# Performance work log

Measured on AMD Instinct MI355X. Metric: run time of the kernel, lower is better.

The kernel has to match this reference:

```python
import jax, jax.numpy as jnp
import numpy as np
import math

DIM = 2048
D_STATE = 64
EXPAND = 2
CHUNK = 64
HEADDIM = 64
D_CONV = 4
D_INNER = EXPAND * DIM          # 4096
NHEADS = D_INNER // HEADDIM     # 64


def _segsum(x):
    """x: (..., T) -> (..., T, T); out[i,j] = sum_{k=j+1}^{i} x[k] for i>=j else -inf."""
    T = x.shape[-1]
    keep = jnp.tril(jnp.ones((T, T), bool), -1)          # strictly lower
    seg = jnp.cumsum(jnp.where(keep, x[..., None], 0.0), axis=-2)
    valid = jnp.tril(jnp.ones((T, T), bool))
    return jnp.where(valid, seg, -jnp.inf)


def _ssd(X, A, B, C, block):
    """Chunkwise SSD scan (Mamba-2 Listing 1). X:(b,L,h,p) A:(b,L,h) B,C:(b,L,h,n)."""
    b, L, h, p = X.shape
    n = B.shape[-1]
    c = L // block
    X = X.reshape(b, c, block, h, p)
    A = A.reshape(b, c, block, h)
    B = B.reshape(b, c, block, h, n)
    C = C.reshape(b, c, block, h, n)
    A = jnp.transpose(A, (0, 3, 1, 2))                    # (b,h,c,l)
    A_cum = jnp.cumsum(A, axis=-1)
    # intra-chunk (diagonal block) output
    L_intra = jnp.exp(_segsum(A))                         # (b,h,c,l,s)
    Y_diag = jnp.einsum('bclhn,bcshn,bhcls,bcshp->bclhp', C, B, L_intra, X)
    # per-chunk final states
    decay_states = jnp.exp(A_cum[..., -1:] - A_cum)       # (b,h,c,l)
    states = jnp.einsum('bclhn,bhcl,bclhp->bchpn', B, decay_states, X)
    states = jnp.concatenate([jnp.zeros_like(states[:, :1]), states], axis=1)
    # inter-chunk recurrence across chunk boundaries
    chunk_end = jnp.pad(A_cum[..., -1], ((0, 0), (0, 0), (1, 0)))  # (b,h,c+1)
    decay_chunk = jnp.exp(_segsum(chunk_end))             # (b,h,c+1,c+1)
    new_states = jnp.einsum('bhzc,bchpn->bzhpn', decay_chunk, states)
    states_per_chunk = new_states[:, :-1]
    # off-diagonal contribution from carried-in states
    state_decay_out = jnp.exp(A_cum)                      # (b,h,c,l)
    Y_off = jnp.einsum('bclhn,bchpn,bhcl->bclhp', C, states_per_chunk, state_decay_out)
    return (Y_diag + Y_off).reshape(b, L, h, p)


def setup_inputs() -> dict:
    key = jax.random.key(0)
    ks = jax.random.split(key, 6)
    b, l = 2, 2048
    x = jax.random.normal(ks[0], (b, l, DIM), jnp.float32)
    proj_out = 2 * D_INNER + 2 * D_STATE + NHEADS
    in_proj_w = jax.random.normal(ks[1], (proj_out, DIM), jnp.float32) / math.sqrt(DIM)
    conv_w = jax.random.normal(ks[2], (D_INNER, 1, D_CONV), jnp.float32) / math.sqrt(D_CONV)
    conv_b = jnp.zeros((D_INNER,), jnp.float32)
    out_proj_w = jax.random.normal(ks[3], (DIM, D_INNER), jnp.float32) / math.sqrt(D_INNER)
    A_log = jnp.zeros((NHEADS,), jnp.float32)
    D_skip = jnp.ones((D_INNER,), jnp.float32)
    u = jax.random.uniform(ks[4], (NHEADS,), jnp.float32)
    dt = jnp.clip(jnp.exp(u * (math.log(0.1) - math.log(0.001)) + math.log(0.001)), 1e-4, None)
    dt_bias = dt + jnp.log(-jnp.expm1(-dt))
    return dict(x=x, in_proj_w=in_proj_w, conv_w=conv_w, conv_b=conv_b,
                out_proj_w=out_proj_w, A_log=A_log, D_skip=D_skip, dt_bias=dt_bias)


def reference(x, in_proj_w, conv_w, conv_b, out_proj_w, A_log, D_skip, dt_bias):
    b, l, _ = x.shape
    proj = x @ in_proj_w.T
    splits = [D_INNER, 2 * D_INNER, 2 * D_INNER + D_STATE, 2 * D_INNER + 2 * D_STATE]
    x_branch, z, B_in, C_in, dt = jnp.split(proj, splits, axis=-1)
    # causal depthwise conv1d (torch pads both sides then slices [:l] == left-pad only)
    xc = jnp.transpose(x_branch, (0, 2, 1))               # (b, d_inner, l)
    xc = jax.lax.conv_general_dilated(
        xc, conv_w, (1,), [(D_CONV - 1, 0)],
        dimension_numbers=('NCH', 'OIH', 'NCH'), feature_group_count=D_INNER)
    xc = xc + conv_b[None, :, None]
    x_act = jax.nn.silu(jnp.transpose(xc, (0, 2, 1)))     # (b,l,d_inner)
    x_h = x_act.reshape(b, l, NHEADS, HEADDIM)
    dt_f = jax.nn.softplus(dt + dt_bias)                  # (b,l,h)
    A_f = -jnp.exp(A_log)                                 # (h,)
    X_disc = x_h * dt_f[..., None]
    A_disc = A_f[None, None, :] * dt_f
    B_b = jnp.broadcast_to(B_in[:, :, None, :], (b, l, NHEADS, D_STATE))
    C_b = jnp.broadcast_to(C_in[:, :, None, :], (b, l, NHEADS, D_STATE))
    Y = _ssd(X_disc, A_disc, B_b, C_b, CHUNK)             # (b,l,h,p)
    y = Y.reshape(b, l, D_INNER) + D_skip * x_act
    y = y * jax.nn.silu(z)
    return y @ out_proj_w.T
```

## Files before the change

### kernel.cpp

```cpp
#include <hip/hip_runtime.h>

typedef unsigned short u16;
typedef unsigned int   u32;
typedef __attribute__((ext_vector_type(8))) short bf16x8;
typedef __attribute__((ext_vector_type(4))) float f32x4;

__device__ __forceinline__ u16 f2bf(float f){
  u32 u = __builtin_bit_cast(u32, f);
  u32 r = (u + 0x7FFFu + ((u >> 16) & 1u)) >> 16;
  return (u16)r;
}
__device__ __forceinline__ float bf2f(u16 h){
  u32 u = ((u32)h) << 16;
  return __builtin_bit_cast(float, u);
}
__device__ __forceinline__ void llds16(const u16* g, u16* l){
  __builtin_amdgcn_global_load_lds((const __attribute__((address_space(1))) void*)g,
                                   (__attribute__((address_space(3))) void*)l, 16, 0, 0);
}

#define FENCE asm volatile("" ::: "memory")
#define BAR   do { FENCE; __builtin_amdgcn_s_barrier(); FENCE; } while (0)
#define LGKM0 do { asm volatile("s_waitcnt lgkmcnt(0)" ::: "memory"); __builtin_amdgcn_sched_barrier(0); } while (0)
#define VMC6  do { asm volatile("s_waitcnt vmcnt(6)" ::: "memory"); __builtin_amdgcn_sched_barrier(0); } while (0)
#define VMC0  do { asm volatile("s_waitcnt vmcnt(0)" ::: "memory"); __builtin_amdgcn_sched_barrier(0); } while (0)

#define MFMAQ(mh, nh)                                                         \
  _Pragma("unroll") for (int i = 0; i < 4; i++)                               \
    _Pragma("unroll") for (int j = 0; j < 2; j++)                             \
      _Pragma("unroll") for (int kb = 0; kb < 2; kb++)                        \
        acc[mh][nh][i][j] = __builtin_amdgcn_mfma_f32_16x16x32_bf16(          \
            a[i][kb], bfr[j][kb], acc[mh][nh][i][j], 0, 0, 0);

__global__ __launch_bounds__(256) void cast4(const float* __restrict__ in, u16* __restrict__ out, int n4){
  int i = blockIdx.x * 256 + threadIdx.x;
  if (i >= n4) return;
  float4 v = ((const float4*)in)[i];
  u32 lo = (u32)f2bf(v.x) | ((u32)f2bf(v.y) << 16);
  u32 hi = (u32)f2bf(v.z) | ((u32)f2bf(v.w) << 16);
  ((uint2*)out)[i] = make_uint2(lo, hi);
}

__global__ __launch_bounds__(256) void castpad_w1(const float* __restrict__ in, u16* __restrict__ out){
  int i = blockIdx.x * 256 + threadIdx.x;
  if (i >= 8448 * 512) return;
  int nrow = i >> 9;
  float4 v = make_float4(0.f, 0.f, 0.f, 0.f);
  if (nrow < 8384) v = ((const float4*)in)[i];
  u32 lo = (u32)f2bf(v.x) | ((u32)f2bf(v.y) << 16);
  u32 hi = (u32)f2bf(v.z) | ((u32)f2bf(v.w) << 16);
  ((uint2*)out)[i] = make_uint2(lo, hi);
}

__global__ __launch_bounds__(256)
void gemm128(const u16* __restrict__ A, const u16* __restrict__ Bm, u16* __restrict__ Cout,
             int NYT, int N, int K)
{
  __shared__ u16 As[8192], Bs[8192];
  const int tid = threadIdx.x;
  const int lane = tid & 63, wave = tid >> 6;
  const int wm = (wave >> 1) * 64, wn = (wave & 1) * 64;
  const int lr = lane & 15, lk8 = (lane >> 4) * 8;
  const int lterm = lr * 32 + (lk8 ^ ((lr & 8) << 1));
  const int nwg = gridDim.x;
  const int lid = blockIdx.x;
  const int q = nwg >> 3;
  const int swz = (lid & 7) * q + (lid >> 3);
  const int ty = swz % NYT, tx = swz / NYT;
  const size_t bm0 = (size_t)ty * 128;
  const size_t bn0 = (size_t)tx * 128;
  const int cg = (lane & 3) ^ ((lane & 32) ? 2 : 0);
  const int rsub = lane >> 2;
  const int ag0 = (wave >> 1) * 8;
  const int bg0 = (wave & 1) * 8;

  f32x4 acc[4][4] = {};

  for (int k0 = 0; k0 < K; k0 += 64) {
    __syncthreads();
    #pragma unroll
    for (int u = 0; u < 4; u++) {
      const int si = wave * 4 + u;
      const int row = (si >> 1) * 16 + rsub;
      const int kc = (si & 1) * 32 + cg * 8;
      llds16(A  + (bm0 + row) * (size_t)K + k0 + kc, As + si * 512 + lane * 8);
      llds16(Bm + (bn0 + row) * (size_t)K + k0 + kc, Bs + si * 512 + lane * 8);
    }
    __syncthreads();
    #pragma unroll
    for (int kb = 0; kb < 2; kb++) {
      bf16x8 af[4], bfv[4];
      #pragma unroll
      for (int m = 0; m < 4; m++) af[m]  = *(const bf16x8*)&As[(ag0 + m * 2 + kb) * 512 + lterm];
      #pragma unroll
      for (int n = 0; n < 4; n++) bfv[n] = *(const bf16x8*)&Bs[(bg0 + n * 2 + kb) * 512 + lterm];
      #pragma unroll
      for (int m = 0; m < 4; m++)
        #pragma unroll
        for (int n = 0; n < 4; n++)
          acc[m][n] = __builtin_amdgcn_mfma_f32_16x16x32_bf16(af[m], bfv[n], acc[m][n], 0, 0, 0);
    }
  }

  const int lg = (lane >> 4) * 4;
  #pragma unroll
  for (int m = 0; m < 4; m++)
    #pragma unroll
    for (int n = 0; n < 4; n++) {
      size_t col = bn0 + wn + n * 16 + lr;
      #pragma unroll
      for (int j = 0; j < 4; j++) {
        size_t row = bm0 + wm + m * 16 + lg + j;
        Cout[row * N + col] = f2bf(acc[m][n][j]);
      }
    }
}

__global__ __launch_bounds__(512, 2)
void gemm2sk(const u16* __restrict__ A, const u16* __restrict__ Bm, float* __restrict__ P,
             int NYT, int N, int KLEN, int LDK)
{
  __shared__ u16 L[65536];
  const int tid = threadIdx.x;
  const int lane = tid & 63, wid = tid >> 6;
  const int wr = wid >> 2, wc = wid & 3;
  const int lr = lane & 15, lk8 = (lane >> 4) * 8;
  const int lterm = lr * 32 + (lk8 ^ ((lr & 8) << 1));
  const int lid = blockIdx.x;
  const int ks = lid >> 7;
  const int lid2 = lid & 127;
  const int q = 128 >> 3;
  const int swz = (lid2 & 7) * q + (lid2 >> 3);
  const int ty = swz % NYT, tx = swz / NYT;
  const size_t bm0 = (size_t)ty * 256;
  const size_t bn0 = (size_t)tx * 256;
  const int NT = KLEN >> 6;
  const size_t koff = (size_t)ks * KLEN;
  float* Pout = P + (size_t)ks * 8388608;

  const int si0 = wid * 2, si1 = si0 + 1;
  const int rsub = lane >> 2;
  const int cg = (lane & 3) ^ ((lane & 32) ? 2 : 0);
  const int rh0 = (si0 >> 1) * 16 + rsub, kc0 = (si0 & 1) * 32 + cg * 8;
  const int rh1 = (si1 >> 1) * 16 + rsub, kc1 = (si1 & 1) * 32 + cg * 8;

  auto stage = [&](int isA, int h, int tt) {
    const int slot = (tt & 1) * 4 + (isA ? 0 : 2) + h;
    const u16* gb = (isA ? A : Bm) + ((isA ? bm0 : bn0) + (size_t)h * 128) * (size_t)LDK + koff;
    u16* lb = L + slot * 8192 + lane * 8;
    llds16(gb + (size_t)rh0 * LDK + (size_t)tt * 64 + kc0, lb + si0 * 512);
    llds16(gb + (size_t)rh1 * LDK + (size_t)tt * 64 + kc1, lb + si1 * 512);
  };

  bf16x8 a[4][2], bfr[2][2];
  f32x4 acc[2][2][4][2] = {};

  auto rdA = [&](int p, int mh) {
    #pragma unroll
    for (int i = 0; i < 4; i++)
      #pragma unroll
      for (int kb = 0; kb < 2; kb++)
        a[i][kb] = *(const bf16x8*)&L[(p * 4 + mh) * 8192 + ((wr * 4 + i) * 2 + kb) * 512 + lterm];
  };
  auto rdB = [&](int p, int nh) {
    #pragma unroll
    for (int j = 0; j < 2; j++)
      #pragma unroll
      for (int kb = 0; kb < 2; kb++)
        bfr[j][kb] = *(const bf16x8*)&L[(p * 4 + 2 + nh) * 8192 + ((wc * 2 + j) * 2 + kb) * 512 + lterm];
  };

  stage(1, 0, 0); stage(1, 1, 0); stage(0, 0, 0); stage(0, 1, 0);
  stage(1, 0, 1); stage(1, 1, 1); stage(0, 0, 1);
  VMC6;
  BAR;

  for (int t = 0; t < NT; ++t) {
    const int p = t & 1;
    const bool s1 = (t + 1 < NT);
    const bool s2 = (t + 2 < NT);
    rdA(p, 0); rdB(p, 0);
    if (s1) stage(0, 1, t + 1);
    BAR; LGKM0;
    __builtin_amdgcn_s_setprio(1); MFMAQ(0, 0); __builtin_amdgcn_s_setprio(0);
    BAR;
    rdB(p, 1);
    if (s2) stage(1, 0, t + 2);
    BAR; LGKM0;
    __builtin_amdgcn_s_setprio(1); MFMAQ(0, 1); __builtin_amdgcn_s_setprio(0);
    BAR;
    rdA(p, 1); rdB(p, 0);
    BAR; LGKM0;
    __builtin_amdgcn_s_setprio(1); MFMAQ(1, 0); __builtin_amdgcn_s_setprio(0);
    BAR;
    rdB(p, 1);
    if (s2) { stage(1, 1, t + 2); stage(0, 0, t + 2); }
    if (t < NT - 2) { VMC6; } else { VMC0; }
    BAR; LGKM0;
    __builtin_amdgcn_s_setprio(1); MFMAQ(1, 1); __builtin_amdgcn_s_setprio(0);
    BAR;
  }

  const int lg4 = (lane >> 4) * 4;
  #pragma unroll
  for (int mh = 0; mh < 2; mh++)
    #pragma unroll
    for (int nh = 0; nh < 2; nh++)
      #pragma unroll
      for (int i = 0; i < 4; i++)
        #pragma unroll
        for (int j = 0; j < 2; j++) {
          size_t col = bn0 + nh * 128 + wc * 32 + j * 16 + lr;
          #pragma unroll
          for (int r2 = 0; r2 < 4; r2++) {
            size_t row = bm0 + mh * 128 + wr * 64 + i * 16 + lg4 + r2;
            Pout[row * N + col] = acc[mh][nh][i][j][r2];
          }
        }
}

__global__ __launch_bounds__(256)
void addp(const float* __restrict__ p0, const float* __restrict__ p1, float* __restrict__ out){
  int i = blockIdx.x * 256 + threadIdx.x;
  float4 a = ((const float4*)p0)[i];
  float4 b = ((const float4*)p1)[i];
  ((float4*)out)[i] = make_float4(a.x + b.x, a.y + b.y, a.z + b.z, a.w + b.w);
}

__global__ __launch_bounds__(256)
void postproj(const u16* __restrict__ proj, const float* __restrict__ dt_bias,
              float* __restrict__ dtf, u16* __restrict__ Bb, u16* __restrict__ Cb)
{
  int i = blockIdx.x * 256 + threadIdx.x;
  if (i >= 4096 * 64) return;
  int bl = i >> 6, hh = i & 63;
  const u16* pr = proj + (size_t)bl * 8448;
  float dv = bf2f(pr[8320 + hh]) + dt_bias[hh];
  dtf[i] = dv > 20.f ? dv : log1pf(__expf(dv));
  Bb[i] = pr[8192 + hh];
  Cb[i] = pr[8256 + hh];
}

__global__ __launch_bounds__(256)
void conv_silu(const u16* __restrict__ proj, const float* __restrict__ cw,
               const float* __restrict__ cb, const float* __restrict__ dtf,
               u16* __restrict__ xact, u16* __restrict__ Xd)
{
  const int g = blockIdx.x;
  const int bl0 = g * 4;
  const int l0 = bl0 & 2047;
  const int d0 = blockIdx.y * 2048 + threadIdx.x * 8;
  const int hd = d0 >> 6;
  float4 wv[8];
  #pragma unroll
  for (int e = 0; e < 8; e++) wv[e] = *(const float4*)&cw[(size_t)(d0 + e) * 4];
  float bias[8];
  {
    float4 b0 = *(const float4*)&cb[d0];
    float4 b1 = *(const float4*)&cb[d0 + 4];
    bias[0]=b0.x; bias[1]=b0.y; bias[2]=b0.z; bias[3]=b0.w;
    bias[4]=b1.x; bias[5]=b1.y; bias[6]=b1.z; bias[7]=b1.w;
  }
  float r[7][8];
  #pragma unroll
  for (int t = 0; t < 7; t++) {
    const int l = l0 - 3 + t;
    if (l >= 0) {
      uint4 rv = *(const uint4*)(proj + (size_t)(bl0 - 3 + t) * 8448 + d0);
      const u16* re = (const u16*)&rv;
      #pragma unroll
      for (int e = 0; e < 8; e++) r[t][e] = bf2f(re[e]);
    } else {
      #pragma unroll
      for (int e = 0; e < 8; e++) r[t][e] = 0.f;
    }
  }
  #pragma unroll
  for (int lo = 0; lo < 4; lo++) {
    const float dt = dtf[(size_t)(bl0 + lo) * 64 + hd];
    u16 xo[8], xdo[8];
    #pragma unroll
    for (int e = 0; e < 8; e++) {
      float v = bias[e] + wv[e].x * r[lo][e] + wv[e].y * r[lo + 1][e]
                        + wv[e].z * r[lo + 2][e] + wv[e].w * r[lo + 3][e];
      float sil = v / (1.f + __expf(-v));
      xo[e]  = f2bf(sil);
      xdo[e] = f2bf(sil * dt);
    }
    *(uint4*)(xact + (size_t)(bl0 + lo) * 4096 + d0) = *(const uint4*)xo;
    *(uint4*)(Xd   + (size_t)(bl0 + lo) * 4096 + d0) = *(const uint4*)xdo;
  }
}

__global__ __launch_bounds__(256)
void ssd_states(const u16* __restrict__ Xd, const u16* __restrict__ Bg,
                const float* __restrict__ dtf, const float* __restrict__ A_log,
                u16* __restrict__ Stg, float* __restrict__ dtot)
{
  const int wg = blockIdx.x;
  const int b = wg >> 11, h = wg & 63;
  const int c = (wg >> 6) & 31;
  const int bl0 = b * 2048 + c * 64;
  __shared__ u16 Bt[64*64], Xts[64*64];
  __shared__ float avals[64], Acum[64], Adec[64];
  const int tid = threadIdx.x, wave = tid >> 6, lane = tid & 63;
  const int qi = (wave >> 1) * 32, qj = (wave & 1) * 32;
  const int lr = lane & 15, lk8 = (lane >> 4) * 8, lg = (lane >> 4) * 4;
  const float negA = -__expf(A_log[h]);

  if (tid < 64) avals[tid] = negA * dtf[(size_t)(bl0 + tid) * 64 + h];
  __syncthreads();
  if (tid < 64) { float s = 0.f; for (int j = 0; j <= tid; j++) s += avals[j]; Acum[tid] = s; }
  __syncthreads();
  if (tid < 64) Adec[tid] = __expf(Acum[63] - Acum[tid]);
  if (tid == 0) dtot[wg] = __expf(Acum[63]);
  __syncthreads();
  {
    int s = tid & 63, c0 = (tid >> 6) * 16;
    float dec = Adec[s];
    const u16* bs = Bg + (size_t)(bl0 + s) * 64 + c0;
    const u16* xs = Xd + (size_t)(bl0 + s) * 4096 + h * 64 + c0;
    #pragma unroll
    for (int j = 0; j < 16; j++) {
      Bt[(c0 + j) * 64 + s] = bs[j];
      Xts[(c0 + j) * 64 + s] = f2bf(bf2f(xs[j]) * dec);
    }
  }
  __syncthreads();
  f32x4 accst[2][2] = {};
  #pragma unroll
  for (int kk = 0; kk < 64; kk += 32) {
    bf16x8 xsf[2], btf[2];
    #pragma unroll
    for (int t = 0; t < 2; t++) {
      xsf[t] = *(const bf16x8*)&Xts[(qi + t * 16 + lr) * 64 + kk + lk8];
      btf[t] = *(const bf16x8*)&Bt [(qj + t * 16 + lr) * 64 + kk + lk8];
    }
    #pragma unroll
    for (int ti = 0; ti < 2; ti++)
      #pragma unroll
      for (int tj = 0; tj < 2; tj++)
        accst[ti][tj] = __builtin_amdgcn_mfma_f32_16x16x32_bf16(xsf[ti], btf[tj], accst[ti][tj], 0, 0, 0);
  }
  u16* So = Stg + (size_t)wg * 4096;
  #pragma unroll
  for (int ti = 0; ti < 2; ti++)
    #pragma unroll
    for (int tj = 0; tj < 2; tj++) {
      int nn = qj + tj * 16 + lr;
      #pragma unroll
      for (int r2 = 0; r2 < 4; r2++) {
        int pp = qi + ti * 16 + lg + r2;
        So[pp * 64 + nn] = f2bf(accst[ti][tj][r2]);
      }
    }
}

__global__ __launch_bounds__(256)
void ssd_scan(u16* __restrict__ Stg, const float* __restrict__ dtot)
{
  const int gid = blockIdx.x * 256 + threadIdx.x;
  const int bh = gid >> 12;
  const int pn = gid & 4095;
  const int b = bh >> 6, h = bh & 63;
  float R = 0.f;
  for (int c = 0; c < 32; ++c) {
    const int whc = b * 2048 + c * 64 + h;
    size_t idx = (size_t)whc * 4096 + pn;
    float st = bf2f(Stg[idx]);
    Stg[idx] = f2bf(R);
    R = R * dtot[whc] + st;
  }
}

__global__ __launch_bounds__(256)
void ssd_y(const u16* __restrict__ Xd, const u16* __restrict__ Bg, const u16* __restrict__ Cg,
           const float* __restrict__ dtf, const float* __restrict__ A_log,
           const u16* __restrict__ xact, const u16* __restrict__ proj,
           const float* __restrict__ Dskip, const u16* __restrict__ Stg,
           u16* __restrict__ Yout)
{
  const int wg = blockIdx.x;
  const int b = wg >> 11, h = wg & 63;
  const int c = (wg >> 6) & 31;
  const int bl0 = b * 2048 + c * 64;
  __shared__ u16 Cb[64*64], Bb[64*64], Xt[64*64], Sb[64*64], P[64*64];
  __shared__ float avals[64], Acum[64], Aexp[64];
  const int tid = threadIdx.x, wave = tid >> 6, lane = tid & 63;
  const int qi = (wave >> 1) * 32, qj = (wave & 1) * 32;
  const int lr = lane & 15, lk8 = (lane >> 4) * 8, lg = (lane >> 4) * 4;
  const float negA = -__expf(A_log[h]);

  if (tid < 64) avals[tid] = negA * dtf[(size_t)(bl0 + tid) * 64 + h];
  __syncthreads();
  if (tid < 64) { float s = 0.f; for (int j = 0; j <= tid; j++) s += avals[j]; Acum[tid] = s; }
  __syncthreads();
  if (tid < 64) Aexp[tid] = __expf(Acum[tid]);
  __syncthreads();
  {
    int l = tid >> 2, n0 = (tid & 3) * 16;
    const uint4* s0 = (const uint4*)(Cg + (size_t)(bl0 + l) * 64 + n0);
    *(uint4*)&Cb[l * 64 + n0] = s0[0]; *(uint4*)&Cb[l * 64 + n0 + 8] = s0[1];
    const uint4* s1 = (const uint4*)(Bg + (size_t)(bl0 + l) * 64 + n0);
    *(uint4*)&Bb[l * 64 + n0] = s1[0]; *(uint4*)&Bb[l * 64 + n0 + 8] = s1[1];
    int s = tid & 63, c0 = (tid >> 6) * 16;
    const u16* xs = Xd + (size_t)(bl0 + s) * 4096 + h * 64 + c0;
    #pragma unroll
    for (int j = 0; j < 16; j++) Xt[(c0 + j) * 64 + s] = xs[j];
    const uint4* sp = (const uint4*)(Stg + (size_t)wg * 4096 + tid * 16);
    *(uint4*)&Sb[tid * 16] = sp[0]; *(uint4*)&Sb[tid * 16 + 8] = sp[1];
  }
  __syncthreads();
  f32x4 accs[2][2] = {}; f32x4 accy[2][2] = {};
  #pragma unroll
  for (int kk = 0; kk < 64; kk += 32) {
    bf16x8 cf[2], bfr[2], sf[2];
    #pragma unroll
    for (int t = 0; t < 2; t++) {
      cf[t]  = *(const bf16x8*)&Cb[(qi + t * 16 + lr) * 64 + kk + lk8];
      bfr[t] = *(const bf16x8*)&Bb[(qj + t * 16 + lr) * 64 + kk + lk8];
      sf[t]  = *(const bf16x8*)&Sb[(qj + t * 16 + lr) * 64 + kk + lk8];
    }
    #pragma unroll
    for (int ti = 0; ti < 2; ti++)
      #pragma unroll
      for (int tj = 0; tj < 2; tj++) {
        accs[ti][tj] = __builtin_amdgcn_mfma_f32_16x16x32_bf16(cf[ti], bfr[tj], accs[ti][tj], 0, 0, 0);
        accy[ti][tj] = __builtin_amdgcn_mfma_f32_16x16x32_bf16(cf[ti], sf[tj],  accy[ti][tj], 0, 0, 0);
      }
  }
  #pragma unroll
  for (int ti = 0; ti < 2; ti++)
    #pragma unroll
    for (int tj = 0; tj < 2; tj++) {
      int j = qj + tj * 16 + lr;
      float Aj = Acum[j];
      #pragma unroll
      for (int r2 = 0; r2 < 4; r2++) {
        int i = qi + ti * 16 + lg + r2;
        float v = (i >= j) ? accs[ti][tj][r2] * __expf(Acum[i] - Aj) : 0.f;
        P[i * 64 + j] = f2bf(v);
        accy[ti][tj][r2] *= Aexp[i];
      }
    }
  __syncthreads();
  #pragma unroll
  for (int kk = 0; kk < 64; kk += 32) {
    bf16x8 pf[2], xf_[2];
    #pragma unroll
    for (int t = 0; t < 2; t++) {
      pf[t]  = *(const bf16x8*)&P [(qi + t * 16 + lr) * 64 + kk + lk8];
      xf_[t] = *(const bf16x8*)&Xt[(qj + t * 16 + lr) * 64 + kk + lk8];
    }
    #pragma unroll
    for (int ti = 0; ti < 2; ti++)
      #pragma unroll
      for (int tj = 0; tj < 2; tj++)
        accy[ti][tj] = __builtin_amdgcn_mfma_f32_16x16x32_bf16(pf[ti], xf_[tj], accy[ti][tj], 0, 0, 0);
  }
  #pragma unroll
  for (int ti = 0; ti < 2; ti++)
    #pragma unroll
    for (int tj = 0; tj < 2; tj++) {
      int pcol = qj + tj * 16 + lr;
      int d = h * 64 + pcol;
      float dsk = Dskip[d];
      #pragma unroll
      for (int r2 = 0; r2 < 4; r2++) {
        int lrow = qi + ti * 16 + lg + r2;
        size_t bl = (size_t)bl0 + lrow;
        float y = accy[ti][tj][r2];
        float xa = bf2f(xact[bl * 4096 + d]);
        float z = bf2f(proj[bl * 8448 + 4096 + d]);
        float sz = z / (1.f + __expf(-z));
        Yout[bl * 4096 + d] = f2bf((y + dsk * xa) * sz);
      }
    }
}

__global__ __launch_bounds__(256)
void ssd_kernel(const u16* __restrict__ Xd, const u16* __restrict__ Bg, const u16* __restrict__ Cg,
                const float* __restrict__ dtf, const float* __restrict__ A_log,
                const u16* __restrict__ xact, const u16* __restrict__ proj,
                const float* __restrict__ Dskip, u16* __restrict__ Yout)
{
  const int bh = blockIdx.x;
  const int b = bh >> 6, h = bh & 63;
  __shared__ float S[64 * 64];
  __shared__ u16 Cb[64*64], Bb[64*64], Bt[64*64], Xt[64*64], Xts[64*64], Sb[64*64], P[64*64];
  __shared__ float avals[64], Acum[64], Adec[64], Aexp[64];
  const int tid = threadIdx.x, wave = tid >> 6, lane = tid & 63;
  const int qi = (wave >> 1) * 32, qj = (wave & 1) * 32;
  const int lr = lane & 15, lk8 = (lane >> 4) * 8, lg = (lane >> 4) * 4;
  const float negA = -__expf(A_log[h]);

  for (int i = tid; i < 4096; i += 256) S[i] = 0.f;

  for (int c = 0; c < 32; ++c) {
    const int bl0 = b * 2048 + c * 64;
    __syncthreads();
    if (tid < 64) avals[tid] = negA * dtf[(size_t)(bl0 + tid) * 64 + h];
    __syncthreads();
    if (tid < 64) { float s = 0.f; for (int j = 0; j <= tid; j++) s += avals[j]; Acum[tid] = s; }
    __syncthreads();
    if (tid < 64) { float At = Acum[63]; Adec[tid] = __expf(At - Acum[tid]); Aexp[tid] = __expf(Acum[tid]); }
    __syncthreads();
    {
      int l = tid >> 2, n0 = (tid & 3) * 16;
      const uint4* s0 = (const uint4*)(Cg + (size_t)(bl0 + l) * 64 + n0);
      *(uint4*)&Cb[l * 64 + n0] = s0[0]; *(uint4*)&Cb[l * 64 + n0 + 8] = s0[1];
      const uint4* s1 = (const uint4*)(Bg + (size_t)(bl0 + l) * 64 + n0);
      *(uint4*)&Bb[l * 64 + n0] = s1[0]; *(uint4*)&Bb[l * 64 + n0 + 8] = s1[1];
      int s = tid & 63, c0 = (tid >> 6) * 16;
      float dec = Adec[s];
      const u16* bs = Bg + (size_t)(bl0 + s) * 64 + c0;
      const u16* xs = Xd + (size_t)(bl0 + s) * 4096 + h * 64 + c0;
      #pragma unroll
      for (int j = 0; j < 16; j++) {
        Bt[(c0 + j) * 64 + s] = bs[j];
        u16 xv = xs[j];
        Xt[(c0 + j) * 64 + s] = xv;
        Xts[(c0 + j) * 64 + s] = f2bf(bf2f(xv) * dec);
      }
      int p = tid >> 2, m0 = (tid & 3) * 16;
      #pragma unroll
      for (int j = 0; j < 16; j++) Sb[p * 64 + m0 + j] = f2bf(S[p * 64 + m0 + j]);
    }
    __syncthreads();
    f32x4 accs[2][2] = {}; f32x4 accy[2][2] = {};
    #pragma unroll
    for (int kk = 0; kk < 64; kk += 32) {
      bf16x8 cf[2], bfr[2], sf[2];
      #pragma unroll
      for (int t = 0; t < 2; t++) {
        cf[t]  = *(const bf16x8*)&Cb[(qi + t * 16 + lr) * 64 + kk + lk8];
        bfr[t] = *(const bf16x8*)&Bb[(qj + t * 16 + lr) * 64 + kk + lk8];
        sf[t]  = *(const bf16x8*)&Sb[(qj + t * 16 + lr) * 64 + kk + lk8];
      }
      #pragma unroll
      for (int ti = 0; ti < 2; ti++)
        #pragma unroll
        for (int tj = 0; tj < 2; tj++) {
          accs[ti][tj] = __builtin_amdgcn_mfma_f32_16x16x32_bf16(cf[ti], bfr[tj], accs[ti][tj], 0, 0, 0);
          accy[ti][tj] = __builtin_amdgcn_mfma_f32_16x16x32_bf16(cf[ti], sf[tj],  accy[ti][tj], 0, 0, 0);
        }
    }
    #pragma unroll
    for (int ti = 0; ti < 2; ti++)
      #pragma unroll
      for (int tj = 0; tj < 2; tj++) {
        int j = qj + tj * 16 + lr;
        float Aj = Acum[j];
        #pragma unroll
        for (int r2 = 0; r2 < 4; r2++) {
          int i = qi + ti * 16 + lg + r2;
          float v = (i >= j) ? accs[ti][tj][r2] * __expf(Acum[i] - Aj) : 0.f;
          P[i * 64 + j] = f2bf(v);
          accy[ti][tj][r2] *= Aexp[i];
        }
      }
    __syncthreads();
    f32x4 accst[2][2] = {};
    #pragma unroll
    for (int kk = 0; kk < 64; kk += 32) {
      bf16x8 pf[2], xf_[2], xsf[2], btf[2];
      #pragma unroll
      for (int t = 0; t < 2; t++) {
        pf[t]  = *(const bf16x8*)&P  [(qi + t * 16 + lr) * 64 + kk + lk8];
        xf_[t] = *(const bf16x8*)&Xt [(qj + t * 16 + lr) * 64 + kk + lk8];
        xsf[t] = *(const bf16x8*)&Xts[(qi + t * 16 + lr) * 64 + kk + lk8];
        btf[t] = *(const bf16x8*)&Bt [(qj + t * 16 + lr) * 64 + kk + lk8];
      }
      #pragma unroll
      for (int ti = 0; ti < 2; ti++)
        #pragma unroll
        for (int tj = 0; tj < 2; tj++) {
          accy[ti][tj]  = __builtin_amdgcn_mfma_f32_16x16x32_bf16(pf[ti],  xf_[tj], accy[ti][tj],  0, 0, 0);
          accst[ti][tj] = __builtin_amdgcn_mfma_f32_16x16x32_bf16(xsf[ti], btf[tj], accst[ti][tj], 0, 0, 0);
        }
    }
    float dtot = Aexp[63];
    #pragma unroll
    for (int ti = 0; ti < 2; ti++)
      #pragma unroll
      for (int tj = 0; tj < 2; tj++) {
        int nn = qj + tj * 16 + lr;
        #pragma unroll
        for (int r2 = 0; r2 < 4; r2++) {
          int pp = qi + ti * 16 + lg + r2;
          int idx = pp * 64 + nn;
          S[idx] = dtot * S[idx] + accst[ti][tj][r2];
        }
      }
    #pragma unroll
    for (int ti = 0; ti < 2; ti++)
      #pragma unroll
      for (int tj = 0; tj < 2; tj++) {
        int pcol = qj + tj * 16 + lr;
        int d = h * 64 + pcol;
        float dsk = Dskip[d];
        #pragma unroll
        for (int r2 = 0; r2 < 4; r2++) {
          int lrow = qi + ti * 16 + lg + r2;
          size_t bl = (size_t)bl0 + lrow;
          float y = accy[ti][tj][r2];
          float xa = bf2f(xact[bl * 4096 + d]);
          float z = bf2f(proj[bl * 8448 + 4096 + d]);
          float sz = z / (1.f + __expf(-z));
          Yout[bl * 4096 + d] = f2bf((y + dsk * xa) * sz);
        }
      }
  }
}

extern "C" void kernel_launch(void* const* d_in, const int* in_sizes, int n_in,
                              void* d_out, int out_size, void* d_ws, size_t ws_size,
                              hipStream_t stream) {
  const float* x    = (const float*)d_in[0];
  const float* w1   = (const float*)d_in[1];
  const float* cw   = (const float*)d_in[2];
  const float* cbv  = (const float*)d_in[3];
  const float* w2   = (const float*)d_in[4];
  const float* alog = (const float*)d_in[5];
  const float* dsk  = (const float*)d_in[6];
  const float* dtb  = (const float*)d_in[7];
  float* out = (float*)d_out;

  char* ws = (char*)d_ws;
  u16*  x_bf  = (u16*)(ws + 0);
  u16*  w1p   = (u16*)(ws + 16777216);
  u16*  w2b   = (u16*)(ws + 51380224);
  u16*  proj  = (u16*)(ws + 68157440);
  float* dtf  = (float*)(ws + 137363456);
  u16*  Bbf   = (u16*)(ws + 138412032);
  u16*  Cbf   = (u16*)(ws + 138936320);
  u16*  xact  = (u16*)(ws + 139460608);
  u16*  Xdd   = (u16*)(ws + 173015040);
  u16*  yin   = (u16*)(ws + 206569472);
  u16*  Stg   = (u16*)(ws + 240123904);
  float* dtot = (float*)(ws + 273678336);
  const size_t NEED_PAR = 273694720ull;
  float* p0 = (float*)(ws + 68157440);
  float* p1 = p0 + 8388608;

  cast4<<<8192, 256, 0, stream>>>(x,  x_bf, 2097152);
  castpad_w1<<<16896, 256, 0, stream>>>(w1, w1p);
  cast4<<<8192, 256, 0, stream>>>(w2, w2b, 2097152);

  gemm128<<<2112, 256, 0, stream>>>(x_bf, w1p, proj, 32, 8448, 2048);

  postproj<<<1024, 256, 0, stream>>>(proj, dtb, dtf, Bbf, Cbf);
  conv_silu<<<dim3(1024, 2), 256, 0, stream>>>(proj, cw, cbv, dtf, xact, Xdd);

  if (ws_size >= NEED_PAR) {
    ssd_states<<<4096, 256, 0, stream>>>(Xdd, Bbf, dtf, alog, Stg, dtot);
    ssd_scan<<<2048, 256, 0, stream>>>(Stg, dtot);
    ssd_y<<<4096, 256, 0, stream>>>(Xdd, Bbf, Cbf, dtf, alog, xact, proj, dsk, Stg, yin);
  } else {
    ssd_kernel<<<128, 256, 0, stream>>>(Xdd, Bbf, Cbf, dtf, alog, xact, proj, dsk, yin);
  }

  gemm2sk<<<256, 512, 0, stream>>>(yin, w2b, p0, 16, 2048, 2048, 4096);
  addp<<<8192, 256, 0, stream>>>(p0, p1, out);
}
```

Before: 395.2 us.

## Replace split-K 256-tile out-proj GEMM and reduction with templated 128-tile GEMM

The output projection used a 256x256-tile split-K kernel writing two fp32 partials, followed by a separate add kernel. It now reuses the 128x128 gemm128 kernel, templated to write fp32 directly, with 512 blocks over the full K=4096. This removes the partial-sum writes, the extra reduction pass and one launch. The trade-off is giving up the larger tile and the more carefully pipelined schedule, with longer per-block K loops.

Result: slower. 413.5 us (+4.6%).

```diff
diff --git a/kernel.cpp b/kernel.cpp
--- a/kernel.cpp
+++ b/kernel.cpp
@@ -18,19 +18,6 @@
   __builtin_amdgcn_global_load_lds((const __attribute__((address_space(1))) void*)g,
                                    (__attribute__((address_space(3))) void*)l, 16, 0, 0);
 }
-
-#define FENCE asm volatile("" ::: "memory")
-#define BAR   do { FENCE; __builtin_amdgcn_s_barrier(); FENCE; } while (0)
-#define LGKM0 do { asm volatile("s_waitcnt lgkmcnt(0)" ::: "memory"); __builtin_amdgcn_sched_barrier(0); } while (0)
-#define VMC6  do { asm volatile("s_waitcnt vmcnt(6)" ::: "memory"); __builtin_amdgcn_sched_barrier(0); } while (0)
-#define VMC0  do { asm volatile("s_waitcnt vmcnt(0)" ::: "memory"); __builtin_amdgcn_sched_barrier(0); } while (0)
-
-#define MFMAQ(mh, nh)                                                         \
-  _Pragma("unroll") for (int i = 0; i < 4; i++)                               \
-    _Pragma("unroll") for (int j = 0; j < 2; j++)                             \
-      _Pragma("unroll") for (int kb = 0; kb < 2; kb++)                        \
-        acc[mh][nh][i][j] = __builtin_amdgcn_mfma_f32_16x16x32_bf16(          \
-            a[i][kb], bfr[j][kb], acc[mh][nh][i][j], 0, 0, 0);
 
 __global__ __launch_bounds__(256) void cast4(const float* __restrict__ in, u16* __restrict__ out, int n4){
   int i = blockIdx.x * 256 + threadIdx.x;
@@ -52,8 +39,9 @@
   ((uint2*)out)[i] = make_uint2(lo, hi);
 }
 
-__global__ __launch_bounds__(256)
-void gemm128(const u16* __restrict__ A, const u16* __restrict__ Bm, u16* __restrict__ Cout,
+template<bool OUTF32>
+__global__ __launch_bounds__(256)
+void gemm128(const u16* __restrict__ A, const u16* __restrict__ Bm, void* __restrict__ Cout,
              int NYT, int N, int K)
 {
   __shared__ u16 As[8192], Bs[8192];
@@ -111,120 +99,11 @@
       #pragma unroll
       for (int j = 0; j < 4; j++) {
         size_t row = bm0 + wm + m * 16 + lg + j;
-        Cout[row * N + col] = f2bf(acc[m][n][j]);
-      }
-    }
-}
-
-__global__ __launch_bounds__(512, 2)
-void gemm2sk(const u16* __restrict__ A, const u16* __restrict__ Bm, float* __restrict__ P,
-             int NYT, int N, int KLEN, int LDK)
-{
-  __shared__ u16 L[65536];
-  const int tid = threadIdx.x;
-  const int lane = tid & 63, wid = tid >> 6;
-  const int wr = wid >> 2, wc = wid & 3;
-  const int lr = lane & 15, lk8 = (lane >> 4) * 8;
-  const int lterm = lr * 32 + (lk8 ^ ((lr & 8) << 1));
-  const int lid = blockIdx.x;
-  const int ks = lid >> 7;
-  const int lid2 = lid & 127;
-  const int q = 128 >> 3;
-  const int swz = (lid2 & 7) * q + (lid2 >> 3);
-  const int ty = swz % NYT, tx = swz / NYT;
-  const size_t bm0 = (size_t)ty * 256;
-  const size_t bn0 = (size_t)tx * 256;
-  const int NT = KLEN >> 6;
-  const size_t koff = (size_t)ks * KLEN;
-  float* Pout = P + (size_t)ks * 8388608;
-
-  const int si0 = wid * 2, si1 = si0 + 1;
-  const int rsub = lane >> 2;
-  const int cg = (lane & 3) ^ ((lane & 32) ? 2 : 0);
-  const int rh0 = (si0 >> 1) * 16 + rsub, kc0 = (si0 & 1) * 32 + cg * 8;
-  const int rh1 = (si1 >> 1) * 16 + rsub, kc1 = (si1 & 1) * 32 + cg * 8;
-
-  auto stage = [&](int isA, int h, int tt) {
-    const int slot = (tt & 1) * 4 + (isA ? 0 : 2) + h;
-    const u16* gb = (isA ? A : Bm) + ((isA ? bm0 : bn0) + (size_t)h * 128) * (size_t)LDK + koff;
-    u16* lb = L + slot * 8192 + lane * 8;
-    llds16(gb + (size_t)rh0 * LDK + (size_t)tt * 64 + kc0, lb + si0 * 512);
-    llds16(gb + (size_t)rh1 * LDK + (size_t)tt * 64 + kc1, lb + si1 * 512);
-  };
-
-  bf16x8 a[4][2], bfr[2][2];
-  f32x4 acc[2][2][4][2] = {};
-
-  auto rdA = [&](int p, int mh) {
-    #pragma unroll
-    for (int i = 0; i < 4; i++)
-      #pragma unroll
-      for (int kb = 0; kb < 2; kb++)
-        a[i][kb] = *(const bf16x8*)&L[(p * 4 + mh) * 8192 + ((wr * 4 + i) * 2 + kb) * 512 + lterm];
-  };
-  auto rdB = [&](int p, int nh) {
-    #pragma unroll
-    for (int j = 0; j < 2; j++)
-      #pragma unroll
-      for (int kb = 0; kb < 2; kb++)
-        bfr[j][kb] = *(const bf16x8*)&L[(p * 4 + 2 + nh) * 8192 + ((wc * 2 + j) * 2 + kb) * 512 + lterm];
-  };
-
-  stage(1, 0, 0); stage(1, 1, 0); stage(0, 0, 0); stage(0, 1, 0);
-  stage(1, 0, 1); stage(1, 1, 1); stage(0, 0, 1);
-  VMC6;
-  BAR;
-
-  for (int t = 0; t < NT; ++t) {
-    const int p = t & 1;
-    const bool s1 = (t + 1 < NT);
-    const bool s2 = (t + 2 < NT);
-    rdA(p, 0); rdB(p, 0);
-    if (s1) stage(0, 1, t + 1);
-    BAR; LGKM0;
-    __builtin_amdgcn_s_setprio(1); MFMAQ(0, 0); __builtin_amdgcn_s_setprio(0);
-    BAR;
-    rdB(p, 1);
-    if (s2) stage(1, 0, t + 2);
-    BAR; LGKM0;
-    __builtin_amdgcn_s_setprio(1); MFMAQ(0, 1); __builtin_amdgcn_s_setprio(0);
-    BAR;
-    rdA(p, 1); rdB(p, 0);
-    BAR; LGKM0;
-    __builtin_amdgcn_s_setprio(1); MFMAQ(1, 0); __builtin_amdgcn_s_setprio(0);
-    BAR;
-    rdB(p, 1);
-    if (s2) { stage(1, 1, t + 2); stage(0, 0, t + 2); }
-    if (t < NT - 2) { VMC6; } else { VMC0; }
-    BAR; LGKM0;
-    __builtin_amdgcn_s_setprio(1); MFMAQ(1, 1); __builtin_amdgcn_s_setprio(0);
-    BAR;
-  }
-
-  const int lg4 = (lane >> 4) * 4;
-  #pragma unroll
-  for (int mh = 0; mh < 2; mh++)
-    #pragma unroll
-    for (int nh = 0; nh < 2; nh++)
-      #pragma unroll
-      for (int i = 0; i < 4; i++)
-        #pragma unroll
-        for (int j = 0; j < 2; j++) {
-          size_t col = bn0 + nh * 128 + wc * 32 + j * 16 + lr;
-          #pragma unroll
-          for (int r2 = 0; r2 < 4; r2++) {
-            size_t row = bm0 + mh * 128 + wr * 64 + i * 16 + lg4 + r2;
-            Pout[row * N + col] = acc[mh][nh][i][j][r2];
-          }
-        }
-}
-
-__global__ __launch_bounds__(256)
-void addp(const float* __restrict__ p0, const float* __restrict__ p1, float* __restrict__ out){
-  int i = blockIdx.x * 256 + threadIdx.x;
-  float4 a = ((const float4*)p0)[i];
-  float4 b = ((const float4*)p1)[i];
-  ((float4*)out)[i] = make_float4(a.x + b.x, a.y + b.y, a.z + b.z, a.w + b.w);
+        float v = acc[m][n][j];
+        if (OUTF32) ((float*)Cout)[row * N + col] = v;
+        else        ((u16*)Cout)[row * N + col] = f2bf(v);
+      }
+    }
 }
 
 __global__ __launch_bounds__(256)
@@ -640,14 +519,12 @@
   u16*  Stg   = (u16*)(ws + 240123904);
   float* dtot = (float*)(ws + 273678336);
   const size_t NEED_PAR = 273694720ull;
-  float* p0 = (float*)(ws + 68157440);
-  float* p1 = p0 + 8388608;
 
   cast4<<<8192, 256, 0, stream>>>(x,  x_bf, 2097152);
   castpad_w1<<<16896, 256, 0, stream>>>(w1, w1p);
   cast4<<<8192, 256, 0, stream>>>(w2, w2b, 2097152);
 
-  gemm128<<<2112, 256, 0, stream>>>(x_bf, w1p, proj, 32, 8448, 2048);
+  gemm128<false><<<2112, 256, 0, stream>>>(x_bf, w1p, proj, 32, 8448, 2048);
 
   postproj<<<1024, 256, 0, stream>>>(proj, dtb, dtf, Bbf, Cbf);
   conv_silu<<<dim3(1024, 2), 256, 0, stream>>>(proj, cw, cbv, dtf, xact, Xdd);
@@ -660,6 +537,5 @@
     ssd_kernel<<<128, 256, 0, stream>>>(Xdd, Bbf, Cbf, dtf, alog, xact, proj, dsk, yin);
   }
 
-  gemm2sk<<<256, 512, 0, stream>>>(yin, w2b, p0, 16, 2048, 2048, 4096);
-  addp<<<8192, 256, 0, stream>>>(p0, p1, out);
-}
+  gemm128<true><<<512, 256, 0, stream>>>(yin, w2b, out, 32, 2048, 4096);
+}
```
